# Kernel tuning notes

Hardware: AMD Instinct MI355X
Metric: run time of the kernel (lower is better)

## Reference

```python
import jax, jax.numpy as jnp
import numpy as np

B, N, C, K = 32, 1024, 14, 9      # graphs, residues/graph, atom channels, kNN
E, H, NC = 128, 128, 25           # embed_size, hidden_size, num_classes
NG = 128                          # gaussians in time embedding (== embed_size)


def _ffn(x, W1, b1, W2, b2):
    # nn.Sequential(SiLU, Linear, SiLU, Linear)
    h = jax.nn.silu(x) @ W1 + b1
    return jax.nn.silu(h) @ W2 + b2


def _time_emb(t, Wt1, bt1, Wt2, bt2):
    # GaussianSmearing(0,1,NG) -> Linear -> ReLU -> Linear
    offset = jnp.linspace(0.0, 1.0, NG)
    coeff = -0.5 / (offset[1] - offset[0]) ** 2
    d = t[..., None] - offset + 1e-6
    g = jnp.exp(coeff * d * d)
    return jax.nn.relu(g @ Wt1 + bt1) @ Wt2 + bt2


def _forward(S, X, t, emb, Wt1, bt1, Wt2, bt2, We1, be1, We2, be2,
             Wx1, bx1, Wx2, bx2, Wh1, bh1, Wh2, bh2,
             Wd1, bd1, Wd2, bd2, Wp1, bp1, Wr1, br1, Wr2, br2):
    H0 = emb[S]                                           # [B,N,E]
    Hh = H0 + _time_emb(t, Wt1, bt1, Wt2, bt2)            # H_0 + time_emb
    # dynamic kNN graph on CA coordinates (channel 1), per graph
    ca = X[:, :, 1]                                       # [B,N,3]
    d2 = jnp.sum((ca[:, :, None] - ca[:, None]) ** 2, -1) # [B,N,N]
    d2 = d2 + jnp.eye(N, dtype=d2.dtype) * 1e10           # no self loops
    _, idx = jax.lax.top_k(-d2, K)                        # [B,N,K] neighbor ids
    gather = jax.vmap(lambda a, i: a[i])                  # per-graph gather
    Xnb = gather(X, idx)                                  # [B,N,K,C,3]
    Hnb = gather(Hh, idx)                                 # [B,N,K,E]
    rel = X[:, :, None] - Xnb                             # [B,N,K,C,3]
    # multi-channel radial features (EGNN-style channel Gram matrix)
    radial = jnp.einsum('bnkcd,bnked->bnkce', rel, rel).reshape(B, N, K, C * C) / C
    Hi = jnp.broadcast_to(Hh[:, :, None], (B, N, K, E))
    m = _ffn(jnp.concatenate([Hi, Hnb, radial], -1), We1, be1, We2, be2)  # [B,N,K,H]
    # EGNN coordinate update
    w = _ffn(m, Wx1, bx1, Wx2, bx2)                       # [B,N,K,1]
    X_out = X + jnp.mean(rel * w[..., None], axis=2)      # [B,N,C,3]
    # node update
    Hn = Hh + _ffn(jnp.concatenate([Hh, jnp.sum(m, 2)], -1), Wh1, bh1, Wh2, bh2)
    # symmetric edge-distance FFN: f([src,dst]) + f([dst,src])
    Hs = jnp.broadcast_to(Hn[:, :, None], (B, N, K, E))
    Hd = gather(Hn, idx)
    pd = (_ffn(jnp.concatenate([Hs, Hd], -1), Wd1, bd1, Wd2, bd2)
          + _ffn(jnp.concatenate([Hd, Hs], -1), Wd1, bd1, Wd2, bd2))[..., 0]  # [B,N,K]
    # pred_logits = ffn_residue2(pre_H_0 * sigmoid(ffn_proj(H)))
    gate = jax.nn.sigmoid(jax.nn.silu(Hn) @ Wp1 + bp1)
    logits = _ffn(H0 * gate, Wr1, br1, Wr2, br2)          # [B,N,NC]
    return logits, X_out, pd


def setup_inputs() -> dict:
    key = jax.random.key(0)
    ks = jax.random.split(key, 34)
    p = lambda k, s: (0.02 * jax.random.normal(k, s)).astype(jnp.float32)
    inp = {
        'X': jax.random.normal(ks[0], (B, N, C, 3), jnp.float32),
        'S': jax.random.randint(ks[1], (B, N), 0, NC),
        't': jax.random.uniform(ks[2], (B, N), jnp.float32),
        'emb': p(ks[3], (NC, E)),
        'Wt1': p(ks[4], (NG, H)), 'bt1': jnp.zeros((H,), jnp.float32),
        'Wt2': p(ks[5], (H, E)), 'bt2': jnp.zeros((E,), jnp.float32),
        'We1': p(ks[6], (2 * E + C * C, H)), 'be1': jnp.zeros((H,), jnp.float32),
        'We2': p(ks[7], (H, H)), 'be2': jnp.zeros((H,), jnp.float32),
        'Wx1': p(ks[8], (H, H)), 'bx1': jnp.zeros((H,), jnp.float32),
        'Wx2': p(ks[9], (H, 1)), 'bx2': jnp.zeros((1,), jnp.float32),
        'Wh1': p(ks[10], (E + H, H)), 'bh1': jnp.zeros((H,), jnp.float32),
        'Wh2': p(ks[11], (H, E)), 'bh2': jnp.zeros((E,), jnp.float32),
        'Wd1': p(ks[12], (2 * E, H)), 'bd1': jnp.zeros((H,), jnp.float32),
        'Wd2': p(ks[13], (H, 1)), 'bd2': jnp.zeros((1,), jnp.float32),
        'Wp1': p(ks[14], (E, E)), 'bp1': jnp.zeros((E,), jnp.float32),
        'Wr1': p(ks[15], (E, H)), 'br1': jnp.zeros((H,), jnp.float32),
        'Wr2': p(ks[16], (H, NC)), 'br2': jnp.zeros((NC,), jnp.float32),
    }
    return inp


def reference(X, S, t, emb, Wt1, bt1, Wt2, bt2, We1, be1, We2, be2,
              Wx1, bx1, Wx2, bx2, Wh1, bh1, Wh2, bh2,
              Wd1, bd1, Wd2, bd2, Wp1, bp1, Wr1, br1, Wr2, br2):
    return _forward(S, X, t, emb, Wt1, bt1, Wt2, bt2, We1, be1, We2, be2,
                    Wx1, bx1, Wx2, bx2, Wh1, bh1, Wh2, bh2,
                    Wd1, bd1, Wd2, bd2, Wp1, bp1, Wr1, br1, Wr2, br2)
```

## Files before the change

### kernel.cpp

```cpp
#include <hip/hip_runtime.h>

#define BATCH 32
#define NPT   1024
#define CC    14
#define KNN   9
#define EDIM  128
#define HDIM  128
#define NCLS  25
#define BN    (BATCH*NPT)

#define RSTR  236
#define SSTR  140

typedef float  v4f __attribute__((ext_vector_type(4)));
typedef __bf16 v8bf __attribute__((ext_vector_type(8)));

__device__ __forceinline__ float silu_f(float x) {
    const float e = __expf(-x);
    return x * __builtin_amdgcn_rcpf(1.0f + e);
}
__device__ __forceinline__ float sigm_f(float x) {
    const float e = __expf(-x);
    return __builtin_amdgcn_rcpf(1.0f + e);
}

__device__ __forceinline__ unsigned short f2bf_rne(float f) {
    union { float f; unsigned u; } v; v.f = f;
    unsigned r = v.u + 0x7fffu + ((v.u >> 16) & 1u);
    return (unsigned short)(r >> 16);
}
__device__ __forceinline__ unsigned short f2bf(float f) {
    union { float f; unsigned u; } v; v.f = f;
    return (unsigned short)((v.u + 0x8000u) >> 16);
}

__global__ __launch_bounds__(256) void k_prep(
    const float* __restrict__ We1, const float* __restrict__ We2,
    const float* __restrict__ Wx1, const float* __restrict__ Wh1,
    const float* __restrict__ Wh2, const float* __restrict__ Wd1,
    const float* __restrict__ Wp1, const float* __restrict__ Wr1,
    const float* __restrict__ Wt1, const float* __restrict__ Wt2,
    unsigned short* __restrict__ WeRt, unsigned short* __restrict__ We2t,
    unsigned short* __restrict__ Wx1t, unsigned short* __restrict__ Wh1t,
    unsigned short* __restrict__ Wh2t, unsigned short* __restrict__ Wd1t,
    unsigned short* __restrict__ Wp1t, unsigned short* __restrict__ Wr1t,
    unsigned short* __restrict__ Wt1t, unsigned short* __restrict__ Wt2t,
    unsigned short* __restrict__ We1Ft)
{
    int i = blockIdx.x * 256 + threadIdx.x;
    if (i < 128*224) {
        const int chan = i / 224, k = i % 224;
        WeRt[i] = (k < 196) ? f2bf_rne(We1[(size_t)(256 + k)*128 + chan]) : (unsigned short)0;
        return;
    }
    i -= 128*224;
    if (i < 16384) { We2t[i] = f2bf_rne(We2[(size_t)(i % 128)*128 + i/128]); return; }
    i -= 16384;
    if (i < 16384) { Wx1t[i] = f2bf_rne(Wx1[(size_t)(i % 128)*128 + i/128]); return; }
    i -= 16384;
    if (i < 32768) { const int c = i/256, k = i%256; Wh1t[i] = f2bf_rne(Wh1[(size_t)k*128 + c]); return; }
    i -= 32768;
    if (i < 16384) { Wh2t[i] = f2bf_rne(Wh2[(size_t)(i % 128)*128 + i/128]); return; }
    i -= 16384;
    if (i < 32768) {
        const int t = i/128, k = i%128;
        Wd1t[i] = f2bf_rne((t < 128) ? Wd1[(size_t)k*128 + t] : Wd1[(size_t)(128 + k)*128 + (t - 128)]);
        return;
    }
    i -= 32768;
    if (i < 16384) { Wp1t[i] = f2bf_rne(Wp1[(size_t)(i % 128)*128 + i/128]); return; }
    i -= 16384;
    if (i < 16384) { Wr1t[i] = f2bf_rne(Wr1[(size_t)(i % 128)*128 + i/128]); return; }
    i -= 16384;
    if (i < 16384) { Wt1t[i] = f2bf_rne(Wt1[(size_t)(i % 128)*128 + i/128]); return; }
    i -= 16384;
    if (i < 16384) { Wt2t[i] = f2bf_rne(Wt2[(size_t)(i % 128)*128 + i/128]); return; }
    i -= 16384;
    if (i < 32768) {
        const int t = i/128, k = i%128;
        We1Ft[i] = f2bf_rne((t < 128) ? We1[(size_t)k*128 + t] : We1[(size_t)(128 + k)*128 + (t - 128)]);
    }
}

__global__ __launch_bounds__(256) void k_hhP(
    const float* __restrict__ t, const int* __restrict__ S,
    const float* __restrict__ emb,
    const unsigned short* __restrict__ Wt1t, const float* __restrict__ bt1,
    const unsigned short* __restrict__ Wt2t, const float* __restrict__ bt2,
    const unsigned short* __restrict__ We1Ft, const float* __restrict__ be1,
    float* __restrict__ Hh, float* __restrict__ P)
{
    __shared__ __align__(16) unsigned short A0[32*140];
    __shared__ __align__(16) unsigned short A1[32*140];
    __shared__ __align__(16) unsigned short A2[32*140];
    __shared__ int sInt[32];

    const int tid  = threadIdx.x;
    const int wv   = tid >> 6, lane = tid & 63;
    const int quad = lane >> 4, r16 = lane & 15;
    const int col  = tid & 127, rh = tid >> 7;
    const int base = blockIdx.x * 32;

    if (tid < 32) sInt[tid] = S[base + tid];

    const float step  = 1.0f / 127.0f;
    const float coeff = -0.5f / (step * step);
    const float off   = step * (float)col;
    #pragma unroll
    for (int rr = 0; rr < 16; ++rr) {
        const int r = rh*16 + rr;
        const float d = t[base + r] - off + 1e-6f;
        A0[r*140 + col] = f2bf(__expf(coeff * d * d));
    }
    __syncthreads();

    {
        v8bf a[2][4];
        #pragma unroll
        for (int g = 0; g < 2; ++g)
            #pragma unroll
            for (int ks = 0; ks < 4; ++ks)
                a[g][ks] = *(const v8bf*)(A0 + (16*g + r16)*140 + ks*32 + quad*8);
        #pragma unroll
        for (int c2 = 0; c2 < 2; ++c2) {
            const int ch = (wv*2 + c2)*16 + r16;
            v4f acc[2] = {(v4f){0,0,0,0}, (v4f){0,0,0,0}};
            #pragma unroll
            for (int ks = 0; ks < 4; ++ks) {
                const v8bf bb = *(const v8bf*)(Wt1t + (size_t)ch*128 + ks*32 + quad*8);
                acc[0] = __builtin_amdgcn_mfma_f32_16x16x32_bf16(a[0][ks], bb, acc[0], 0, 0, 0);
                acc[1] = __builtin_amdgcn_mfma_f32_16x16x32_bf16(a[1][ks], bb, acc[1], 0, 0, 0);
            }
            const float bc = bt1[ch];
            #pragma unroll
            for (int g = 0; g < 2; ++g)
                #pragma unroll
                for (int rr = 0; rr < 4; ++rr)
                    A1[(16*g + quad*4 + rr)*140 + ch] = f2bf(fmaxf(acc[g][rr] + bc, 0.0f));
        }
    }
    __syncthreads();

    {
        v8bf a[2][4];
        #pragma unroll
        for (int g = 0; g < 2; ++g)
            #pragma unroll
            for (int ks = 0; ks < 4; ++ks)
                a[g][ks] = *(const v8bf*)(A1 + (16*g + r16)*140 + ks*32 + quad*8);
        #pragma unroll
        for (int c2 = 0; c2 < 2; ++c2) {
            const int ch = (wv*2 + c2)*16 + r16;
            v4f acc[2] = {(v4f){0,0,0,0}, (v4f){0,0,0,0}};
            #pragma unroll
            for (int ks = 0; ks < 4; ++ks) {
                const v8bf bb = *(const v8bf*)(Wt2t + (size_t)ch*128 + ks*32 + quad*8);
                acc[0] = __builtin_amdgcn_mfma_f32_16x16x32_bf16(a[0][ks], bb, acc[0], 0, 0, 0);
                acc[1] = __builtin_amdgcn_mfma_f32_16x16x32_bf16(a[1][ks], bb, acc[1], 0, 0, 0);
            }
            const float bc = bt2[ch];
            #pragma unroll
            for (int g = 0; g < 2; ++g)
                #pragma unroll
                for (int rr = 0; rr < 4; ++rr) {
                    const int row = 16*g + quad*4 + rr;
                    const int node = base + row;
                    const float hh = emb[sInt[row]*128 + ch] + acc[g][rr] + bc;
                    Hh[(size_t)node*128 + ch] = hh;
                    A2[row*140 + ch] = f2bf(silu_f(hh));
                }
        }
    }
    __syncthreads();

    {
        v8bf a[2][4];
        #pragma unroll
        for (int g = 0; g < 2; ++g)
            #pragma unroll
            for (int ks = 0; ks < 4; ++ks)
                a[g][ks] = *(const v8bf*)(A2 + (16*g + r16)*140 + ks*32 + quad*8);
        #pragma unroll
        for (int c2 = 0; c2 < 4; ++c2) {
            const int ch = (wv*4 + c2)*16 + r16;
            v4f acc[2] = {(v4f){0,0,0,0}, (v4f){0,0,0,0}};
            #pragma unroll
            for (int ks = 0; ks < 4; ++ks) {
                const v8bf bb = *(const v8bf*)(We1Ft + (size_t)ch*128 + ks*32 + quad*8);
                acc[0] = __builtin_amdgcn_mfma_f32_16x16x32_bf16(a[0][ks], bb, acc[0], 0, 0, 0);
                acc[1] = __builtin_amdgcn_mfma_f32_16x16x32_bf16(a[1][ks], bb, acc[1], 0, 0, 0);
            }
            const float fb = (ch < 128) ? be1[ch] : 0.0f;
            #pragma unroll
            for (int g = 0; g < 2; ++g)
                #pragma unroll
                for (int rr = 0; rr < 4; ++rr)
                    P[(size_t)(base + 16*g + quad*4 + rr)*256 + ch] = acc[g][rr] + fb;
        }
    }
}

__global__ __launch_bounds__(256) void k_knn(
    const float* __restrict__ X, int* __restrict__ idxb)
{
    __shared__ __align__(16) float4 Cc[NPT];
    __shared__ float dsh[4][64][KNN];
    __shared__ int   ish[4][64][KNN];

    const int tid = threadIdx.x, lane = tid & 63, wv = tid >> 6;
    const int bb = blockIdx.x >> 4;
    const int n0 = (blockIdx.x & 15) << 6;
    const float* Xb = X + (size_t)bb * NPT * 42;

    for (int i = tid; i < NPT; i += 256) {
        const float* p = Xb + (size_t)i*42 + 3;
        Cc[i] = make_float4(p[0], p[1], p[2], 0.0f);
    }
    __syncthreads();

    const int n = n0 + lane;
    const float4 c = Cc[n];

    float dist[KNN]; int ind[KNN];
    #pragma unroll
    for (int k = 0; k < KNN; ++k) { dist[k] = 3.0e38f; ind[k] = -1; }

    const int j0 = wv * 256;
    for (int jj = 0; jj < 256; ++jj) {
        const int j = j0 + jj;
        const float4 q = Cc[j];
        const float dx = __fsub_rn(c.x, q.x);
        const float dy = __fsub_rn(c.y, q.y);
        const float dz = __fsub_rn(c.z, q.z);
        float d = __fadd_rn(__fadd_rn(__fmul_rn(dx,dx), __fmul_rn(dy,dy)), __fmul_rn(dz,dz));
        if (j == n) d = __fadd_rn(d, 1e10f);
        if (d < dist[KNN-1]) {
            dist[KNN-1] = d; ind[KNN-1] = j;
            #pragma unroll
            for (int p = KNN-1; p > 0; --p) {
                if (dist[p] < dist[p-1]) {
                    float td = dist[p]; dist[p] = dist[p-1]; dist[p-1] = td;
                    int   ti = ind[p];  ind[p]  = ind[p-1];  ind[p-1]  = ti;
                }
            }
        }
    }
    #pragma unroll
    for (int k = 0; k < KNN; ++k) { dsh[wv][lane][k] = dist[k]; ish[wv][lane][k] = ind[k]; }
    __syncthreads();

    if (tid < 64) {
        float fd[KNN]; int fi[KNN];
        #pragma unroll
        for (int k = 0; k < KNN; ++k) { fd[k] = 3.0e38f; fi[k] = -1; }
        for (int w = 0; w < 4; ++w)
            #pragma unroll
            for (int k = 0; k < KNN; ++k) {
                const float d = dsh[w][tid][k];
                const int   i = ish[w][tid][k];
                if (d < fd[KNN-1]) {
                    fd[KNN-1] = d; fi[KNN-1] = i;
                    #pragma unroll
                    for (int p = KNN-1; p > 0; --p) {
                        if (fd[p] < fd[p-1]) {
                            float td = fd[p]; fd[p] = fd[p-1]; fd[p-1] = td;
                            int   ti = fi[p]; fi[p] = fi[p-1]; fi[p-1] = ti;
                        }
                    }
                }
            }
        const int node = (bb << 10) + n0 + tid;
        #pragma unroll
        for (int k = 0; k < KNN; ++k) idxb[(size_t)node*KNN + k] = fi[k];
    }
}

__global__ __launch_bounds__(256) void k_edge(
    const float* __restrict__ X, const int* __restrict__ idxb,
    const float* __restrict__ P,
    const unsigned short* __restrict__ WeRt,
    const unsigned short* __restrict__ We2t,
    const unsigned short* __restrict__ Wx1t,
    const float* __restrict__ be2,
    const float* __restrict__ bx1, const float* __restrict__ Wx2,
    const float* __restrict__ bx2,
    float* __restrict__ msum, float* __restrict__ wbuf)
{
    __shared__ unsigned short radF[16*RSTR];
    __shared__ unsigned short silA[16*SSTR];
    __shared__ unsigned short silB[16*SSTR];
    __shared__ __align__(16) float relS[16][57];
    __shared__ float wred[KNN][16][4];
    __shared__ int   jsh[16][KNN];

    const int tid  = threadIdx.x;
    const int wv   = tid >> 6, lane = tid & 63;
    const int quad = lane >> 4, r16 = lane & 15;
    const int node0 = blockIdx.x * 16;
    const int b     = node0 >> 10;
    const int chan0 = (wv*2 + 0)*16 + r16;
    const int chan1 = (wv*2 + 1)*16 + r16;
    const int srow  = tid >> 4, c16 = tid & 15;

    if (tid < 144) jsh[tid/9][tid%9] = idxb[(size_t)(node0 + tid/9)*KNN + tid%9];

    float xr[3] = {0,0,0};
    if (c16 < 14) {
        #pragma unroll
        for (int k = 0; k < 3; ++k)
            xr[k] = X[(size_t)(node0 + srow)*42 + c16*3 + k];
    }

    float pn0[4], pn1[4];
    #pragma unroll
    for (int rr = 0; rr < 4; ++rr) {
        pn0[rr] = P[(size_t)(node0 + quad*4 + rr)*256 + chan0];
        pn1[rr] = P[(size_t)(node0 + quad*4 + rr)*256 + chan1];
    }
    const float be2c0 = be2[chan0], be2c1 = be2[chan1];
    const float bxc0  = bx1[chan0], bxc1  = bx1[chan1];
    const float wxc0  = Wx2[chan0], wxc1  = Wx2[chan1];

    v8bf B1[2][7], B2[2][4], B3[2][4];
    #pragma unroll
    for (int c2 = 0; c2 < 2; ++c2) {
        const int ct = wv*2 + c2;
        #pragma unroll
        for (int ks = 0; ks < 7; ++ks)
            B1[c2][ks] = *(const v8bf*)(WeRt + (size_t)(ct*16 + r16)*224 + ks*32 + quad*8);
        #pragma unroll
        for (int ks = 0; ks < 4; ++ks) {
            B2[c2][ks] = *(const v8bf*)(We2t + (size_t)(ct*16 + r16)*128 + ks*32 + quad*8);
            B3[c2][ks] = *(const v8bf*)(Wx1t + (size_t)(ct*16 + r16)*128 + ks*32 + quad*8);
        }
    }

    float msA0[4] = {0,0,0,0}, msA1[4] = {0,0,0,0};

    __syncthreads();

    float xj[3] = {0,0,0};
    if (c16 < 14) {
        const int j = jsh[srow][0];
        #pragma unroll
        for (int k = 0; k < 3; ++k)
            xj[k] = X[(size_t)((b << 10) + j)*42 + c16*3 + k];
    }

    for (int t = 0; t < KNN; ++t) {
        if (c16 < 14) {
            #pragma unroll
            for (int k = 0; k < 3; ++k)
                relS[srow][c16*4 + k] = xr[k] - xj[k];
        }
        if (t + 1 < KNN && c16 < 14) {
            const int j = jsh[srow][t+1];
            #pragma unroll
            for (int k = 0; k < 3; ++k)
                xj[k] = X[(size_t)((b << 10) + j)*42 + c16*3 + k];
        }
        float pj0[4], pj1[4];
        #pragma unroll
        for (int rr = 0; rr < 4; ++rr) {
            const int jq = jsh[quad*4 + rr][t];
            const size_t jrow = (size_t)((b << 10) + jq)*256 + 128;
            pj0[rr] = P[jrow + chan0];
            pj1[rr] = P[jrow + chan1];
        }

        {
            const float* rb = relS[srow];
            #pragma unroll
            for (int kk = 0; kk < 14; ++kk) {
                const int f = c16 + 16*kk;
                if (f < 196) {
                    const int cI = f / 14, eI = f % 14;
                    const float v = (rb[cI*4]*rb[eI*4] + rb[cI*4+1]*rb[eI*4+1]
                                   + rb[cI*4+2]*rb[eI*4+2]) * (1.0f/14.0f);
                    radF[srow*RSTR + f] = f2bf(silu_f(v));
                } else {
                    radF[srow*RSTR + f] = 0;
                }
            }
        }
        __syncthreads();

        v4f acc10 = (v4f){0,0,0,0}, acc11 = (v4f){0,0,0,0};
        #pragma unroll
        for (int ks = 0; ks < 7; ++ks) {
            const v8bf a = *(const v8bf*)(radF + r16*RSTR + ks*32 + quad*8);
            acc10 = __builtin_amdgcn_mfma_f32_16x16x32_bf16(a, B1[0][ks], acc10, 0, 0, 0);
            acc11 = __builtin_amdgcn_mfma_f32_16x16x32_bf16(a, B1[1][ks], acc11, 0, 0, 0);
        }
        #pragma unroll
        for (int rr = 0; rr < 4; ++rr) {
            const int rw = quad*4 + rr;
            silA[rw*SSTR + chan0] = f2bf(silu_f(acc10[rr] + pn0[rr] + pj0[rr]));
            silA[rw*SSTR + chan1] = f2bf(silu_f(acc11[rr] + pn1[rr] + pj1[rr]));
        }
        __syncthreads();

        v4f acc20 = (v4f){0,0,0,0}, acc21 = (v4f){0,0,0,0};
        #pragma unroll
        for (int ks = 0; ks < 4; ++ks) {
            const v8bf a = *(const v8bf*)(silA + r16*SSTR + ks*32 + quad*8);
            acc20 = __builtin_amdgcn_mfma_f32_16x16x32_bf16(a, B2[0][ks], acc20, 0, 0, 0);
            acc21 = __builtin_amdgcn_mfma_f32_16x16x32_bf16(a, B2[1][ks], acc21, 0, 0, 0);
        }
        #pragma unroll
        for (int rr = 0; rr < 4; ++rr) {
            const float m0 = acc20[rr] + be2c0;
            const float m1 = acc21[rr] + be2c1;
            msA0[rr] += m0;  msA1[rr] += m1;
            const int rw = quad*4 + rr;
            silB[rw*SSTR + chan0] = f2bf(silu_f(m0));
            silB[rw*SSTR + chan1] = f2bf(silu_f(m1));
        }
        __syncthreads();

        v4f acc30 = (v4f){0,0,0,0}, acc31 = (v4f){0,0,0,0};
        #pragma unroll
        for (int ks = 0; ks < 4; ++ks) {
            const v8bf a = *(const v8bf*)(silB + r16*SSTR + ks*32 + quad*8);
            acc30 = __builtin_amdgcn_mfma_f32_16x16x32_bf16(a, B3[0][ks], acc30, 0, 0, 0);
            acc31 = __builtin_amdgcn_mfma_f32_16x16x32_bf16(a, B3[1][ks], acc31, 0, 0, 0);
        }
        #pragma unroll
        for (int rr = 0; rr < 4; ++rr) {
            float pr = silu_f(acc30[rr] + bxc0) * wxc0
                     + silu_f(acc31[rr] + bxc1) * wxc1;
            pr += __shfl_xor(pr, 1);
            pr += __shfl_xor(pr, 2);
            pr += __shfl_xor(pr, 4);
            pr += __shfl_xor(pr, 8);
            if (r16 == 0) wred[t][quad*4 + rr][wv] = pr;
        }
    }

    #pragma unroll
    for (int rr = 0; rr < 4; ++rr) {
        msum[(size_t)(node0 + quad*4 + rr)*128 + chan0] = msA0[rr];
        msum[(size_t)(node0 + quad*4 + rr)*128 + chan1] = msA1[rr];
    }
    __syncthreads();
    if (tid < 16*KNN) {
        const int tt = tid / 16, rw = tid % 16;
        wbuf[(size_t)(node0 + rw)*KNN + tt] =
            wred[tt][rw][0] + wred[tt][rw][1] + wred[tt][rw][2] + wred[tt][rw][3] + bx2[0];
    }
}

__global__ __launch_bounds__(256) void k_nodeF(
    const float* __restrict__ X, const float* __restrict__ Hh,
    const float* __restrict__ msum, const int* __restrict__ idxb,
    const float* __restrict__ wbuf,
    const unsigned short* __restrict__ Wh1t, const float* __restrict__ bh1,
    const unsigned short* __restrict__ Wh2t, const float* __restrict__ bh2,
    const unsigned short* __restrict__ Wd1t, const float* __restrict__ bd1,
    const int* __restrict__ S, const float* __restrict__ emb,
    const unsigned short* __restrict__ Wp1t, const float* __restrict__ bp1,
    const unsigned short* __restrict__ Wr1t, const float* __restrict__ br1,
    const float* __restrict__ Wr2, const float* __restrict__ br2,
    float* __restrict__ Hn, float* __restrict__ AB,
    float* __restrict__ outL, float* __restrict__ outX)
{
    __shared__ __align__(16) unsigned short A0[32*268];
    __shared__ __align__(16) unsigned short A1[32*140];
    __shared__ __align__(16) unsigned short A2[32*140];
    __shared__ __align__(16) unsigned short A3[32*140];
    __shared__ int sInt[32];
    float* A4 = (float*)A0;

    const int tid  = threadIdx.x;
    const int wv   = tid >> 6, lane = tid & 63;
    const int quad = lane >> 4, r16 = lane & 15;
    const int base = blockIdx.x * 32;

    if (tid < 32) sInt[tid] = S[base + tid];
    for (int r = 0; r < 32; ++r) {
        const int node = base + r;
        const float v = (tid < 128) ? Hh[(size_t)node*128 + tid]
                                    : msum[(size_t)node*128 + (tid - 128)];
        A0[r*268 + tid] = f2bf(silu_f(v));
    }
    __syncthreads();

    {
        v8bf a[2][8];
        #pragma unroll
        for (int g = 0; g < 2; ++g)
            #pragma unroll
            for (int ks = 0; ks < 8; ++ks)
                a[g][ks] = *(const v8bf*)(A0 + (16*g + r16)*268 + ks*32 + quad*8);
        #pragma unroll
        for (int c2 = 0; c2 < 2; ++c2) {
            const int ch = (wv*2 + c2)*16 + r16;
            v4f acc[2] = {(v4f){0,0,0,0}, (v4f){0,0,0,0}};
            #pragma unroll
            for (int ks = 0; ks < 8; ++ks) {
                const v8bf bb = *(const v8bf*)(Wh1t + (size_t)ch*256 + ks*32 + quad*8);
                acc[0] = __builtin_amdgcn_mfma_f32_16x16x32_bf16(a[0][ks], bb, acc[0], 0, 0, 0);
                acc[1] = __builtin_amdgcn_mfma_f32_16x16x32_bf16(a[1][ks], bb, acc[1], 0, 0, 0);
            }
            const float bc = bh1[ch];
            #pragma unroll
            for (int g = 0; g < 2; ++g)
                #pragma unroll
                for (int rr = 0; rr < 4; ++rr)
                    A1[(16*g + quad*4 + rr)*140 + ch] = f2bf(silu_f(acc[g][rr] + bc));
        }
    }
    __syncthreads();

    {
        v8bf a[2][4];
        #pragma unroll
        for (int g = 0; g < 2; ++g)
            #pragma unroll
            for (int ks = 0; ks < 4; ++ks)
                a[g][ks] = *(const v8bf*)(A1 + (16*g + r16)*140 + ks*32 + quad*8);
        #pragma unroll
        for (int c2 = 0; c2 < 2; ++c2) {
            const int ch = (wv*2 + c2)*16 + r16;
            v4f acc[2] = {(v4f){0,0,0,0}, (v4f){0,0,0,0}};
            #pragma unroll
            for (int ks = 0; ks < 4; ++ks) {
                const v8bf bb = *(const v8bf*)(Wh2t + (size_t)ch*128 + ks*32 + quad*8);
                acc[0] = __builtin_amdgcn_mfma_f32_16x16x32_bf16(a[0][ks], bb, acc[0], 0, 0, 0);
                acc[1] = __builtin_amdgcn_mfma_f32_16x16x32_bf16(a[1][ks], bb, acc[1], 0, 0, 0);
            }
            const float bc = bh2[ch];
            #pragma unroll
            for (int g = 0; g < 2; ++g)
                #pragma unroll
                for (int rr = 0; rr < 4; ++rr) {
                    const int row = 16*g + quad*4 + rr;
                    const int node = base + row;
                    const float hn = Hh[(size_t)node*128 + ch] + acc[g][rr] + bc;
                    Hn[(size_t)node*128 + ch] = hn;
                    A2[row*140 + ch] = f2bf(silu_f(hn));
                }
        }
    }
    __syncthreads();

    {
        v8bf a[2][4];
        #pragma unroll
        for (int g = 0; g < 2; ++g)
            #pragma unroll
            for (int ks = 0; ks < 4; ++ks)
                a[g][ks] = *(const v8bf*)(A2 + (16*g + r16)*140 + ks*32 + quad*8);

        #pragma unroll
        for (int c2 = 0; c2 < 4; ++c2) {
            const int ch = (wv*4 + c2)*16 + r16;
            v4f acc[2] = {(v4f){0,0,0,0}, (v4f){0,0,0,0}};
            #pragma unroll
            for (int ks = 0; ks < 4; ++ks) {
                const v8bf bb = *(const v8bf*)(Wd1t + (size_t)ch*128 + ks*32 + quad*8);
                acc[0] = __builtin_amdgcn_mfma_f32_16x16x32_bf16(a[0][ks], bb, acc[0], 0, 0, 0);
                acc[1] = __builtin_amdgcn_mfma_f32_16x16x32_bf16(a[1][ks], bb, acc[1], 0, 0, 0);
            }
            const float fb = (ch < 128) ? bd1[ch] : 0.0f;
            #pragma unroll
            for (int g = 0; g < 2; ++g)
                #pragma unroll
                for (int rr = 0; rr < 4; ++rr)
                    AB[(size_t)(base + 16*g + quad*4 + rr)*256 + ch] = acc[g][rr] + fb;
        }

        #pragma unroll
        for (int c2 = 0; c2 < 2; ++c2) {
            const int ch = (wv*2 + c2)*16 + r16;
            v4f acc[2] = {(v4f){0,0,0,0}, (v4f){0,0,0,0}};
            #pragma unroll
            for (int ks = 0; ks < 4; ++ks) {
                const v8bf bb = *(const v8bf*)(Wp1t + (size_t)ch*128 + ks*32 + quad*8);
                acc[0] = __builtin_amdgcn_mfma_f32_16x16x32_bf16(a[0][ks], bb, acc[0], 0, 0, 0);
                acc[1] = __builtin_amdgcn_mfma_f32_16x16x32_bf16(a[1][ks], bb, acc[1], 0, 0, 0);
            }
            const float bc = bp1[ch];
            #pragma unroll
            for (int g = 0; g < 2; ++g)
                #pragma unroll
                for (int rr = 0; rr < 4; ++rr) {
                    const int row = 16*g + quad*4 + rr;
                    const float gg = sigm_f(acc[g][rr] + bc);
                    const float x = emb[sInt[row]*128 + ch] * gg;
                    A3[row*140 + ch] = f2bf(silu_f(x));
                }
        }
    }
    __syncthreads();

    {
        v8bf a[2][4];
        #pragma unroll
        for (int g = 0; g < 2; ++g)
            #pragma unroll
            for (int ks = 0; ks < 4; ++ks)
                a[g][ks] = *(const v8bf*)(A3 + (16*g + r16)*140 + ks*32 + quad*8);
        #pragma unroll
        for (int c2 = 0; c2 < 2; ++c2) {
            const int ch = (wv*2 + c2)*16 + r16;
            v4f acc[2] = {(v4f){0,0,0,0}, (v4f){0,0,0,0}};
            #pragma unroll
            for (int ks = 0; ks < 4; ++ks) {
                const v8bf bb = *(const v8bf*)(Wr1t + (size_t)ch*128 + ks*32 + quad*8);
                acc[0] = __builtin_amdgcn_mfma_f32_16x16x32_bf16(a[0][ks], bb, acc[0], 0, 0, 0);
                acc[1] = __builtin_amdgcn_mfma_f32_16x16x32_bf16(a[1][ks], bb, acc[1], 0, 0, 0);
            }
            const float bc = br1[ch];
            #pragma unroll
            for (int g = 0; g < 2; ++g)
                #pragma unroll
                for (int rr = 0; rr < 4; ++rr)
                    A4[(16*g + quad*4 + rr)*134 + ch] = silu_f(acc[g][rr] + bc);
        }
    }
    __syncthreads();

    for (int o = tid; o < 32*NCLS; o += 256) {
        const int r = o / NCLS, j = o % NCLS;
        float s = 0.0f;
        for (int i = 0; i < 128; ++i) s += A4[r*134 + i] * Wr2[i*NCLS + j];
        outL[(size_t)(base + r)*NCLS + j] = s + br2[j];
    }

    for (int o = tid; o < 32*CC*3; o += 256) {
        const int r = o / (CC*3), q = o % (CC*3);
        const int node = base + r;
        const int bq = node >> 10;
        const int cq = q / 3, dc = q % 3;
        const float xv = X[((size_t)node*CC + cq)*3 + dc];
        float a = 0.0f;
        for (int k = 0; k < KNN; ++k) {
            const int j = idxb[(size_t)node*KNN + k];
            const float xjv = X[(((size_t)(bq << 10) + j)*CC + cq)*3 + dc];
            a += (xv - xjv) * wbuf[(size_t)node*KNN + k];
        }
        outX[(size_t)node*CC*3 + q] = xv + a / 9.0f;
    }
}

__global__ __launch_bounds__(256) void k_pd2(
    const float* __restrict__ AB, const int* __restrict__ idxb,
    const float* __restrict__ Wd2, const float* __restrict__ bd2,
    float* __restrict__ outPd)
{
    const int tid  = threadIdx.x;
    const int lane = tid & 63, wv = tid >> 6;
    const int c0   = lane, c1 = lane + 64;
    const float w0 = Wd2[c0], w1 = Wd2[c1];
    const float b2 = 2.0f * bd2[0];

    #pragma unroll
    for (int s = 0; s < 2; ++s) {
        const int node = blockIdx.x * 8 + wv*2 + s;
        const int b    = node >> 10;

        int jv = 0;
        if (lane < KNN) jv = idxb[(size_t)node*KNN + lane];

        const float An0 = AB[(size_t)node*256 + c0];
        const float An1 = AB[(size_t)node*256 + c1];
        const float Bn0 = AB[(size_t)node*256 + 128 + c0];
        const float Bn1 = AB[(size_t)node*256 + 128 + c1];

        float Aj0[KNN], Aj1[KNN], Bj0[KNN], Bj1[KNN];
        #pragma unroll
        for (int e = 0; e < KNN; ++e) {
            const size_t jn = (size_t)((b << 10) + __shfl(jv, e)) * 256;
            Aj0[e] = AB[jn + c0];       Aj1[e] = AB[jn + c1];
            Bj0[e] = AB[jn + 128 + c0]; Bj1[e] = AB[jn + 128 + c1];
        }
        #pragma unroll
        for (int e = 0; e < KNN; ++e) {
            float p = (silu_f(An0 + Bj0[e]) + silu_f(Aj0[e] + Bn0)) * w0
                    + (silu_f(An1 + Bj1[e]) + silu_f(Aj1[e] + Bn1)) * w1;
            #pragma unroll
            for (int off = 32; off; off >>= 1) p += __shfl_xor(p, off, 64);
            if (lane == 0) outPd[(size_t)node*KNN + e] = p + b2;
        }
    }
}

extern "C" void kernel_launch(void* const* d_in, const int* in_sizes, int n_in,
                              void* d_out, int out_size, void* d_ws, size_t ws_size,
                              hipStream_t stream)
{
    const float* X   = (const float*)d_in[0];
    const int*   S   = (const int*)  d_in[1];
    const float* t   = (const float*)d_in[2];
    const float* emb = (const float*)d_in[3];
    const float* Wt1 = (const float*)d_in[4];
    const float* bt1 = (const float*)d_in[5];
    const float* Wt2 = (const float*)d_in[6];
    const float* bt2 = (const float*)d_in[7];
    const float* We1 = (const float*)d_in[8];
    const float* be1 = (const float*)d_in[9];
    const float* We2 = (const float*)d_in[10];
    const float* be2 = (const float*)d_in[11];
    const float* Wx1 = (const float*)d_in[12];
    const float* bx1 = (const float*)d_in[13];
    const float* Wx2 = (const float*)d_in[14];
    const float* bx2 = (const float*)d_in[15];
    const float* Wh1 = (const float*)d_in[16];
    const float* bh1 = (const float*)d_in[17];
    const float* Wh2 = (const float*)d_in[18];
    const float* bh2 = (const float*)d_in[19];
    const float* Wd1 = (const float*)d_in[20];
    const float* bd1 = (const float*)d_in[21];
    const float* Wd2 = (const float*)d_in[22];
    const float* bd2 = (const float*)d_in[23];
    const float* Wp1 = (const float*)d_in[24];
    const float* bp1 = (const float*)d_in[25];
    const float* Wr1 = (const float*)d_in[26];
    const float* br1 = (const float*)d_in[27];
    const float* Wr2 = (const float*)d_in[28];
    const float* br2 = (const float*)d_in[29];

    float* out   = (float*)d_out;
    float* outL  = out;
    float* outX  = out + (size_t)BN*NCLS;
    float* outPd = outX + (size_t)BN*CC*3;

    unsigned short* WeRt  = (unsigned short*)d_ws;
    unsigned short* We2t  = WeRt  + 28672;
    unsigned short* Wx1t  = We2t  + 16384;
    unsigned short* Wh1t  = Wx1t  + 16384;
    unsigned short* Wh2t  = Wh1t  + 32768;
    unsigned short* Wd1t  = Wh2t  + 16384;
    unsigned short* Wp1t  = Wd1t  + 32768;
    unsigned short* Wr1t  = Wp1t  + 16384;
    unsigned short* Wt1t  = Wr1t  + 16384;
    unsigned short* Wt2t  = Wt1t  + 16384;
    unsigned short* We1Ft = Wt2t  + 16384;
    float* Hh   = (float*)(We1Ft + 32768);
    float* msum = Hh   + (size_t)BN*EDIM;
    float* Hn   = msum + (size_t)BN*HDIM;
    float* wbuf = Hn   + (size_t)BN*EDIM;
    float* P    = wbuf + (size_t)BN*KNN;
    int*   idxb = (int*)(P + (size_t)BN*256);

    k_prep  <<<944,    256, 0, stream>>>(We1, We2, Wx1, Wh1, Wh2, Wd1, Wp1, Wr1, Wt1, Wt2,
                                         WeRt, We2t, Wx1t, Wh1t, Wh2t, Wd1t, Wp1t, Wr1t,
                                         Wt1t, Wt2t, We1Ft);
    k_hhP   <<<BN/32,  256, 0, stream>>>(t, S, emb, Wt1t, bt1, Wt2t, bt2, We1Ft, be1, Hh, P);
    k_knn   <<<BN/64,  256, 0, stream>>>(X, idxb);
    k_edge  <<<BN/16,  256, 0, stream>>>(X, idxb, P, WeRt, We2t, Wx1t,
                                         be2, bx1, Wx2, bx2, msum, wbuf);
    k_nodeF <<<BN/32,  256, 0, stream>>>(X, Hh, msum, idxb, wbuf,
                                         Wh1t, bh1, Wh2t, bh2, Wd1t, bd1,
                                         S, emb, Wp1t, bp1, Wr1t, br1, Wr2, br2,
                                         Hn, P, outL, outX);
    k_pd2   <<<BN/8,   256, 0, stream>>>(P, idxb, Wd2, bd2, outPd);
}
```

Before: 476.3 us.

## Fold symmetric radial Gram features into 105 unique terms, MFMA final logits

The channel Gram matrix is symmetric, and SiLU is applied elementwise. So the edge MLP's first-layer weights for radial features are pre-summed over the (c,e) and (e,c) pairs in the prep kernel. This cuts the radial feature width from 196 (padded 224) to 105 (padded 128), reducing feature computation, LDS traffic and MFMA K-steps in the edge kernel from 7 to 4. Separately, the final Wr2 projection is moved from a scalar fp32 loop to a bf16 MFMA using a transposed, padded Wr2 copy. That last layer now runs in reduced precision, so logits may differ slightly.

```diff
diff --git a/kernel.cpp b/kernel.cpp
--- a/kernel.cpp
+++ b/kernel.cpp
@@ -9,11 +9,42 @@
 #define NCLS  25
 #define BN    (BATCH*NPT)
 
-#define RSTR  236
+#define RSTR  132
 #define SSTR  140
 
 typedef float  v4f __attribute__((ext_vector_type(4)));
 typedef __bf16 v8bf __attribute__((ext_vector_type(8)));
+
+__device__ const unsigned char PC_tab[105] = {
+    0,0,0,0,0,0,0,0,0,0,0,0,0,0,
+    1,1,1,1,1,1,1,1,1,1,1,1,1,
+    2,2,2,2,2,2,2,2,2,2,2,2,
+    3,3,3,3,3,3,3,3,3,3,3,
+    4,4,4,4,4,4,4,4,4,4,
+    5,5,5,5,5,5,5,5,5,
+    6,6,6,6,6,6,6,6,
+    7,7,7,7,7,7,7,
+    8,8,8,8,8,8,
+    9,9,9,9,9,
+    10,10,10,10,
+    11,11,11,
+    12,12,
+    13};
+__device__ const unsigned char PE_tab[105] = {
+    0,1,2,3,4,5,6,7,8,9,10,11,12,13,
+    1,2,3,4,5,6,7,8,9,10,11,12,13,
+    2,3,4,5,6,7,8,9,10,11,12,13,
+    3,4,5,6,7,8,9,10,11,12,13,
+    4,5,6,7,8,9,10,11,12,13,
+    5,6,7,8,9,10,11,12,13,
+    6,7,8,9,10,11,12,13,
+    7,8,9,10,11,12,13,
+    8,9,10,11,12,13,
+    9,10,11,12,13,
+    10,11,12,13,
+    11,12,13,
+    12,13,
+    13};
 
 __device__ __forceinline__ float silu_f(float x) {
     const float e = __expf(-x);
@@ -40,20 +71,27 @@
     const float* __restrict__ Wh2, const float* __restrict__ Wd1,
     const float* __restrict__ Wp1, const float* __restrict__ Wr1,
     const float* __restrict__ Wt1, const float* __restrict__ Wt2,
-    unsigned short* __restrict__ WeRt, unsigned short* __restrict__ We2t,
+    const float* __restrict__ Wr2,
+    unsigned short* __restrict__ WeF,  unsigned short* __restrict__ We2t,
     unsigned short* __restrict__ Wx1t, unsigned short* __restrict__ Wh1t,
     unsigned short* __restrict__ Wh2t, unsigned short* __restrict__ Wd1t,
     unsigned short* __restrict__ Wp1t, unsigned short* __restrict__ Wr1t,
     unsigned short* __restrict__ Wt1t, unsigned short* __restrict__ Wt2t,
-    unsigned short* __restrict__ We1Ft)
+    unsigned short* __restrict__ We1Ft, unsigned short* __restrict__ Wr2t)
 {
     int i = blockIdx.x * 256 + threadIdx.x;
-    if (i < 128*224) {
-        const int chan = i / 224, k = i % 224;
-        WeRt[i] = (k < 196) ? f2bf_rne(We1[(size_t)(256 + k)*128 + chan]) : (unsigned short)0;
+    if (i < 16384) {
+        const int ch = i >> 7, k = i & 127;
+        float v = 0.0f;
+        if (k < 105) {
+            const int c = PC_tab[k], e = PE_tab[k];
+            v = We1[(size_t)(256 + c*14 + e)*128 + ch];
+            if (c != e) v += We1[(size_t)(256 + e*14 + c)*128 + ch];
+        }
+        WeF[i] = f2bf_rne(v);
         return;
     }
-    i -= 128*224;
+    i -= 16384;
     if (i < 16384) { We2t[i] = f2bf_rne(We2[(size_t)(i % 128)*128 + i/128]); return; }
     i -= 16384;
     if (i < 16384) { Wx1t[i] = f2bf_rne(Wx1[(size_t)(i % 128)*128 + i/128]); return; }
@@ -79,6 +117,12 @@
     if (i < 32768) {
         const int t = i/128, k = i%128;
         We1Ft[i] = f2bf_rne((t < 128) ? We1[(size_t)k*128 + t] : We1[(size_t)(128 + k)*128 + (t - 128)]);
+        return;
+    }
+    i -= 32768;
+    if (i < 4096) {
+        const int ch = i >> 7, k = i & 127;
+        Wr2t[i] = (ch < NCLS) ? f2bf_rne(Wr2[(size_t)k*NCLS + ch]) : (unsigned short)0;
     }
 }
 
@@ -278,7 +322,7 @@
 __global__ __launch_bounds__(256) void k_edge(
     const float* __restrict__ X, const int* __restrict__ idxb,
     const float* __restrict__ P,
-    const unsigned short* __restrict__ WeRt,
+    const unsigned short* __restrict__ WeF,
     const unsigned short* __restrict__ We2t,
     const unsigned short* __restrict__ Wx1t,
     const float* __restrict__ be2,
@@ -304,6 +348,19 @@
 
     if (tid < 144) jsh[tid/9][tid%9] = idxb[(size_t)(node0 + tid/9)*KNN + tid%9];
 
+    int offCE[7];
+    #pragma unroll
+    for (int kk = 0; kk < 7; ++kk) {
+        const int f = c16 + 16*kk;
+        if (f < 105) offCE[kk] = ((int)PC_tab[f]*4) | (((int)PE_tab[f]*4) << 16);
+        else         offCE[kk] = 0;
+    }
+    {
+        const int f6 = 96 + c16, f7 = 112 + c16;
+        if (f6 >= 105) radF[srow*RSTR + f6] = 0;
+        radF[srow*RSTR + f7] = 0;
+    }
+
     float xr[3] = {0,0,0};
     if (c16 < 14) {
         #pragma unroll
@@ -321,15 +378,13 @@
     const float bxc0  = bx1[chan0], bxc1  = bx1[chan1];
     const float wxc0  = Wx2[chan0], wxc1  = Wx2[chan1];
 
-    v8bf B1[2][7], B2[2][4], B3[2][4];
+    v8bf B1[2][4], B2[2][4], B3[2][4];
     #pragma unroll
     for (int c2 = 0; c2 < 2; ++c2) {
         const int ct = wv*2 + c2;
         #pragma unroll
-        for (int ks = 0; ks < 7; ++ks)
-            B1[c2][ks] = *(const v8bf*)(WeRt + (size_t)(ct*16 + r16)*224 + ks*32 + quad*8);
-        #pragma unroll
         for (int ks = 0; ks < 4; ++ks) {
+            B1[c2][ks] = *(const v8bf*)(WeF  + (size_t)(ct*16 + r16)*128 + ks*32 + quad*8);
             B2[c2][ks] = *(const v8bf*)(We2t + (size_t)(ct*16 + r16)*128 + ks*32 + quad*8);
             B3[c2][ks] = *(const v8bf*)(Wx1t + (size_t)(ct*16 + r16)*128 + ks*32 + quad*8);
         }
@@ -371,15 +426,13 @@
         {
             const float* rb = relS[srow];
             #pragma unroll
-            for (int kk = 0; kk < 14; ++kk) {
+            for (int kk = 0; kk < 7; ++kk) {
                 const int f = c16 + 16*kk;
-                if (f < 196) {
-                    const int cI = f / 14, eI = f % 14;
-                    const float v = (rb[cI*4]*rb[eI*4] + rb[cI*4+1]*rb[eI*4+1]
-                                   + rb[cI*4+2]*rb[eI*4+2]) * (1.0f/14.0f);
+                if (f < 105) {
+                    const int oc = offCE[kk] & 0xffff, oe = offCE[kk] >> 16;
+                    const float v = (rb[oc]*rb[oe] + rb[oc+1]*rb[oe+1]
+                                   + rb[oc+2]*rb[oe+2]) * (1.0f/14.0f);
                     radF[srow*RSTR + f] = f2bf(silu_f(v));
-                } else {
-                    radF[srow*RSTR + f] = 0;
                 }
             }
         }
@@ -387,7 +440,7 @@
 
         v4f acc10 = (v4f){0,0,0,0}, acc11 = (v4f){0,0,0,0};
         #pragma unroll
-        for (int ks = 0; ks < 7; ++ks) {
+        for (int ks = 0; ks < 4; ++ks) {
             const v8bf a = *(const v8bf*)(radF + r16*RSTR + ks*32 + quad*8);
             acc10 = __builtin_amdgcn_mfma_f32_16x16x32_bf16(a, B1[0][ks], acc10, 0, 0, 0);
             acc11 = __builtin_amdgcn_mfma_f32_16x16x32_bf16(a, B1[1][ks], acc11, 0, 0, 0);
@@ -460,7 +513,7 @@
     const int* __restrict__ S, const float* __restrict__ emb,
     const unsigned short* __restrict__ Wp1t, const float* __restrict__ bp1,
     const unsigned short* __restrict__ Wr1t, const float* __restrict__ br1,
-    const float* __restrict__ Wr2, const float* __restrict__ br2,
+    const unsigned short* __restrict__ Wr2t, const float* __restrict__ br2,
     float* __restrict__ Hn, float* __restrict__ AB,
     float* __restrict__ outL, float* __restrict__ outX)
 {
@@ -469,7 +522,6 @@
     __shared__ __align__(16) unsigned short A2[32*140];
     __shared__ __align__(16) unsigned short A3[32*140];
     __shared__ int sInt[32];
-    float* A4 = (float*)A0;
 
     const int tid  = threadIdx.x;
     const int wv   = tid >> 6, lane = tid & 63;
@@ -616,16 +668,30 @@
             for (int g = 0; g < 2; ++g)
                 #pragma unroll
                 for (int rr = 0; rr < 4; ++rr)
-                    A4[(16*g + quad*4 + rr)*134 + ch] = silu_f(acc[g][rr] + bc);
-        }
-    }
-    __syncthreads();
-
-    for (int o = tid; o < 32*NCLS; o += 256) {
-        const int r = o / NCLS, j = o % NCLS;
-        float s = 0.0f;
-        for (int i = 0; i < 128; ++i) s += A4[r*134 + i] * Wr2[i*NCLS + j];
-        outL[(size_t)(base + r)*NCLS + j] = s + br2[j];
+                    A1[(16*g + quad*4 + rr)*140 + ch] = f2bf(silu_f(acc[g][rr] + bc));
+        }
+    }
+    __syncthreads();
+
+    {
+        const int g = wv >> 1, ct = wv & 1;
+        v8bf a[4];
+        #pragma unroll
+        for (int ks = 0; ks < 4; ++ks)
+            a[ks] = *(const v8bf*)(A1 + (16*g + r16)*140 + ks*32 + quad*8);
+        v4f acc = (v4f){0,0,0,0};
+        #pragma unroll
+        for (int ks = 0; ks < 4; ++ks) {
+            const v8bf bb = *(const v8bf*)(Wr2t + (size_t)(ct*16 + r16)*128 + ks*32 + quad*8);
+            acc = __builtin_amdgcn_mfma_f32_16x16x32_bf16(a[ks], bb, acc, 0, 0, 0);
+        }
+        const int col = ct*16 + r16;
+        if (col < NCLS) {
+            const float bc = br2[col];
+            #pragma unroll
+            for (int rr = 0; rr < 4; ++rr)
+                outL[(size_t)(base + 16*g + quad*4 + rr)*NCLS + col] = acc[rr] + bc;
+        }
     }
 
     for (int o = tid; o < 32*CC*3; o += 256) {
@@ -726,8 +792,8 @@
     float* outX  = out + (size_t)BN*NCLS;
     float* outPd = outX + (size_t)BN*CC*3;
 
-    unsigned short* WeRt  = (unsigned short*)d_ws;
-    unsigned short* We2t  = WeRt  + 28672;
+    unsigned short* WeF   = (unsigned short*)d_ws;
+    unsigned short* We2t  = WeF   + 16384;
     unsigned short* Wx1t  = We2t  + 16384;
     unsigned short* Wh1t  = Wx1t  + 16384;
     unsigned short* Wh2t  = Wh1t  + 32768;
@@ -737,23 +803,24 @@
     unsigned short* Wt1t  = Wr1t  + 16384;
     unsigned short* Wt2t  = Wt1t  + 16384;
     unsigned short* We1Ft = Wt2t  + 16384;
-    float* Hh   = (float*)(We1Ft + 32768);
+    unsigned short* Wr2t  = We1Ft + 32768;
+    float* Hh   = (float*)(Wr2t + 4096);
     float* msum = Hh   + (size_t)BN*EDIM;
     float* Hn   = msum + (size_t)BN*HDIM;
     float* wbuf = Hn   + (size_t)BN*EDIM;
     float* P    = wbuf + (size_t)BN*KNN;
     int*   idxb = (int*)(P + (size_t)BN*256);
 
-    k_prep  <<<944,    256, 0, stream>>>(We1, We2, Wx1, Wh1, Wh2, Wd1, Wp1, Wr1, Wt1, Wt2,
-                                         WeRt, We2t, Wx1t, Wh1t, Wh2t, Wd1t, Wp1t, Wr1t,
-                                         Wt1t, Wt2t, We1Ft);
+    k_prep  <<<912,    256, 0, stream>>>(We1, We2, Wx1, Wh1, Wh2, Wd1, Wp1, Wr1, Wt1, Wt2, Wr2,
+                                         WeF, We2t, Wx1t, Wh1t, Wh2t, Wd1t, Wp1t, Wr1t,
+                                         Wt1t, Wt2t, We1Ft, Wr2t);
     k_hhP   <<<BN/32,  256, 0, stream>>>(t, S, emb, Wt1t, bt1, Wt2t, bt2, We1Ft, be1, Hh, P);
     k_knn   <<<BN/64,  256, 0, stream>>>(X, idxb);
-    k_edge  <<<BN/16,  256, 0, stream>>>(X, idxb, P, WeRt, We2t, Wx1t,
+    k_edge  <<<BN/16,  256, 0, stream>>>(X, idxb, P, WeF, We2t, Wx1t,
                                          be2, bx1, Wx2, bx2, msum, wbuf);
     k_nodeF <<<BN/32,  256, 0, stream>>>(X, Hh, msum, idxb, wbuf,
                                          Wh1t, bh1, Wh2t, bh2, Wd1t, bd1,
-                                         S, emb, Wp1t, bp1, Wr1t, br1, Wr2, br2,
+                                         S, emb, Wp1t, bp1, Wr1t, br1, Wr2t, br2,
                                          Hn, P, outL, outX);
     k_pd2   <<<BN/8,   256, 0, stream>>>(P, idxb, Wd2, bd2, outPd);
 }
```

New measurement: 421.8 us. 11.4% less time.
